# Performance work log

Hardware: AMD Instinct MI355X
Metric: run time of the kernel (lower is better)

Reference implementation:

```python
import jax, jax.numpy as jnp
import numpy as np

ROUTING_ITERS = 3
EPS = 1e-9


def squash(s):
    # s: [..., D]; faithful to the torch code: x / (1 + n^2) / sqrt(n^2 + eps)
    sq = jnp.sum(s * s, axis=-1, keepdims=True)
    return s / (1.0 + sq) / jnp.sqrt(sq + EPS)


def setup_inputs() -> dict:
    key = jax.random.key(0)
    k1, k2 = jax.random.split(key)
    B, I, C, D, d = 64, 4096, 32, 16, 16
    x = jax.random.normal(k1, (B, I, d), dtype=jnp.float32)
    weights = jax.random.normal(k2, (1, I, C, D, d), dtype=jnp.float32)
    return {"x": x, "weights": weights}


def reference(x, weights):
    # u_hat[b,i,c,D] = weights[0,i,c,D,d] @ x[b,i,d]
    u_hat = jnp.einsum('icDd,bid->bicD', weights[0], x)  # [B, I, C, D]
    B, I, C, D = u_hat.shape
    b_ij = jnp.zeros((B, I, C), dtype=u_hat.dtype)
    v_j = None
    for _ in range(ROUTING_ITERS):
        c_ij = jax.nn.softmax(b_ij, axis=2)                     # [B, I, C]
        s_j = jnp.einsum('bic,bicD->bcD', c_ij, u_hat)          # [B, C, D]
        v_j = squash(s_j)                                       # [B, C, D]
        b_ij = b_ij + jnp.einsum('bicD,bcD->bic', u_hat, v_j)   # agreement
    return v_j
```

## Files before the change

kernel.cpp:

```cpp
#include <hip/hip_runtime.h>
#include <math.h>

#define ITILES 256
#define IPB    16

typedef __bf16 bf16x8 __attribute__((ext_vector_type(8)));
typedef float  f32x16 __attribute__((ext_vector_type(16)));

__device__ inline unsigned short f2bf(float f) {
    unsigned int x = __float_as_uint(f);
    x += 0x7fff + ((x >> 16) & 1);
    return (unsigned short)(x >> 16);
}
__device__ inline float bf2f(unsigned short u) {
    return __uint_as_float(((unsigned int)u) << 16);
}
__device__ inline uint4 pack8(const unsigned short* o) {
    uint4 p;
    p.x = o[0] | ((unsigned)o[1] << 16);
    p.y = o[2] | ((unsigned)o[3] << 16);
    p.z = o[4] | ((unsigned)o[5] << 16);
    p.w = o[6] | ((unsigned)o[7] << 16);
    return p;
}

__device__ inline unsigned cvtpk(float lo, float hi) {
    unsigned r;
    asm("v_cvt_pk_bf16_f32 %0, %1, %2" : "=v"(r) : "v"(lo), "v"(hi));
    return r;
}
__device__ inline unsigned split3(float x, float y, unsigned& q2, unsigned& q3) {
    unsigned q1 = cvtpk(x, y);
    float f1x = __uint_as_float(q1 << 16);
    float f1y = __uint_as_float(q1 & 0xffff0000u);
    float rx = x - f1x, ry = y - f1y;
    q2 = cvtpk(rx, ry);
    float f2x = __uint_as_float(q2 << 16);
    float f2y = __uint_as_float(q2 & 0xffff0000u);
    q3 = cvtpk(rx - f2x, ry - f2y);
    return q1;
}

__global__ __launch_bounds__(128) void prep_x(const float* __restrict__ x,
                                              unsigned short* __restrict__ Xp)
{
    const int i = blockIdx.x;
    const int t = threadIdx.x;
    const int b = t >> 1, kh = t & 1;
    const float4* s4 = (const float4*)(x + ((size_t)b * 4096 + i) * 16 + kh * 8);
    float4 wa = s4[0], wb = s4[1];
    float wv[8] = {wa.x, wa.y, wa.z, wa.w, wb.x, wb.y, wb.z, wb.w};
    unsigned short o1[8], o2[8], o3[8];
    #pragma unroll
    for (int j = 0; j < 8; ++j) {
        float w = wv[j];
        o1[j] = f2bf(w);            float f1 = bf2f(o1[j]);
        o2[j] = f2bf(w - f1);       float f2 = bf2f(o2[j]);
        o3[j] = f2bf(w - f1 - f2);
    }
    unsigned short* dst = Xp + (size_t)i * 3072 + kh * 1536 + b * 8;
    *(uint4*)(dst)        = pack8(o1);
    *(uint4*)(dst + 512)  = pack8(o2);
    *(uint4*)(dst + 1024) = pack8(o3);
}

template<int USE_V>
__global__ __launch_bounds__(1024, 4)
void pass_kernel(const float* __restrict__ W,
                 const unsigned short* __restrict__ Xp,
                 const float* __restrict__ vg,
                 float* __restrict__ slab)
{
    __shared__ float4 vt[8192];
    __shared__ float  p_lds[32 * 65];
    __shared__ float  cij_lds[32 * 65];

    const int tid   = threadIdx.x;
    const int mt    = tid >> 6;
    const int lane  = tid & 63;
    const int l31   = lane & 31;
    const int h     = lane >> 5;
    const int cA    = 2 * mt + h;
    const int itile = blockIdx.x;
    const int i0    = itile * IPB;

    const int cW = 2 * mt + ((l31 >> 2) & 1);
    const int DW = (l31 & 3) + 4 * (l31 >> 3);
    const float4* w4 = (const float4*)(W + (size_t)i0 * 8192 + ((cW * 16 + DW) * 16 + h * 8));

    if (USE_V) {
        const float4* v4 = (const float4*)vg;
        #pragma unroll
        for (int k = 0; k < 8; ++k) {
            int idx = k * 1024 + tid;
            int b = idx >> 7, cd = idx & 127;
            vt[b * 128 + (cd ^ (b & 31))] = v4[idx];
        }
        __syncthreads();
    }

    f32x16 s0, s1;
    #pragma unroll
    for (int q = 0; q < 16; ++q) { s0[q] = 0.f; s1[q] = 0.f; }

    float4 wa = w4[0], wb = w4[1];

    for (int ii = 0; ii < IPB; ++ii) {
        const int i = i0 + ii;
        const unsigned short* bb = Xp + (size_t)i * 3072 + (size_t)h * 1536 + l31 * 8;

        uint4 b10 = *(const uint4*)(bb);
        uint4 b11 = *(const uint4*)(bb + 256);

        uint4 a1, a2, a3;
        a1.x = split3(wa.x, wa.y, a2.x, a3.x);
        a1.y = split3(wa.z, wa.w, a2.y, a3.y);
        a1.z = split3(wb.x, wb.y, a2.z, a3.z);
        a1.w = split3(wb.z, wb.w, a2.w, a3.w);

        {
            const int iin = (ii + 1 < IPB) ? (ii + 1) : ii;
            wa = w4[(size_t)iin * 2048];
            wb = w4[(size_t)iin * 2048 + 1];
        }

        #define MF(A_, B_, C_) __builtin_amdgcn_mfma_f32_32x32x16_bf16( \
            __builtin_bit_cast(bf16x8, A_), __builtin_bit_cast(bf16x8, B_), C_, 0, 0, 0)

        if (USE_V == 0) {
            s0 = MF(a1, b10, s0); s1 = MF(a1, b11, s1);
            uint4 b20 = *(const uint4*)(bb + 512);
            uint4 b21 = *(const uint4*)(bb + 512 + 256);
            s0 = MF(a2, b10, s0); s1 = MF(a2, b11, s1);
            uint4 b30 = *(const uint4*)(bb + 1024);
            uint4 b31 = *(const uint4*)(bb + 1024 + 256);
            s0 = MF(a1, b20, s0); s1 = MF(a1, b21, s1);
            s0 = MF(a3, b10, s0); s1 = MF(a3, b11, s1);
            s0 = MF(a2, b20, s0); s1 = MF(a2, b21, s1);
            s0 = MF(a1, b30, s0); s1 = MF(a1, b31, s1);
        } else {
            f32x16 u0, u1;
            #pragma unroll
            for (int q = 0; q < 16; ++q) { u0[q] = 0.f; u1[q] = 0.f; }
            u0 = MF(a1, b10, u0); u1 = MF(a1, b11, u1);
            uint4 b20 = *(const uint4*)(bb + 512);
            uint4 b21 = *(const uint4*)(bb + 512 + 256);
            u0 = MF(a2, b10, u0); u1 = MF(a2, b11, u1);
            uint4 b30 = *(const uint4*)(bb + 1024);
            uint4 b31 = *(const uint4*)(bb + 1024 + 256);
            u0 = MF(a1, b20, u0); u1 = MF(a1, b21, u1);
            u0 = MF(a3, b10, u0); u1 = MF(a3, b11, u1);
            u0 = MF(a2, b20, u0); u1 = MF(a2, b21, u1);
            u0 = MF(a1, b30, u0); u1 = MF(a1, b31, u1);

            #pragma unroll
            for (int nt = 0; nt < 2; ++nt) {
                const f32x16& uu = nt ? u1 : u0;
                const int b = nt * 32 + l31;
                float p = 0.f;
                #pragma unroll
                for (int dblk = 0; dblk < 4; ++dblk) {
                    float4 vv = vt[b * 128 + ((cA * 4 + dblk) ^ l31)];
                    p = fmaf(uu[dblk * 4 + 0], vv.x, p);
                    p = fmaf(uu[dblk * 4 + 1], vv.y, p);
                    p = fmaf(uu[dblk * 4 + 2], vv.z, p);
                    p = fmaf(uu[dblk * 4 + 3], vv.w, p);
                }
                p_lds[cA * 65 + b] = p;
            }
            __syncthreads();
            #pragma unroll
            for (int r2 = 0; r2 < 2; ++r2) {
                const int b = mt * 4 + r2 * 2 + h;
                float e = __expf(p_lds[l31 * 65 + b]);
                float t = e;
                t += __shfl_xor(t, 16); t += __shfl_xor(t, 8);
                t += __shfl_xor(t, 4);  t += __shfl_xor(t, 2);
                t += __shfl_xor(t, 1);
                cij_lds[l31 * 65 + b] = __fdividef(e, t);
            }
            __syncthreads();
            #pragma unroll
            for (int nt = 0; nt < 2; ++nt) {
                const f32x16& uu = nt ? u1 : u0;
                f32x16&       ss = nt ? s1 : s0;
                const int b = nt * 32 + l31;
                const float cij = cij_lds[cA * 65 + b];
                #pragma unroll
                for (int q = 0; q < 16; ++q) ss[q] = fmaf(cij, uu[q], ss[q]);
            }
        }
        #undef MF
    }

    float4* slab4 = (float4*)slab;
    #pragma unroll
    for (int nt = 0; nt < 2; ++nt) {
        const f32x16& ss = nt ? s1 : s0;
        const int b = nt * 32 + l31;
        size_t base = ((size_t)itile * 64 + b) * 128 + cA * 4;
        #pragma unroll
        for (int dblk = 0; dblk < 4; ++dblk) {
            float4 o = {ss[dblk * 4 + 0], ss[dblk * 4 + 1], ss[dblk * 4 + 2], ss[dblk * 4 + 3]};
            slab4[base + dblk] = o;
        }
    }
}

__global__ __launch_bounds__(256)
void reduce_squash(const float* __restrict__ slab, float* __restrict__ out, float scale,
                   const float* __restrict__ v1in, float* __restrict__ vsum)
{
    __shared__ float part[128];
    const int tid  = threadIdx.x;
    const int half = tid >> 7;
    const int o    = blockIdx.x * 128 + (tid & 127);
    float a[8];
    #pragma unroll
    for (int k = 0; k < 8; ++k) a[k] = 0.f;
    for (int g = 0; g < 16; ++g) {
        #pragma unroll
        for (int k = 0; k < 8; ++k)
            a[k] += slab[(size_t)(half * 128 + g * 8 + k) * 32768 + o];
    }
    float s = 0.f;
    #pragma unroll
    for (int k = 0; k < 8; ++k) s += a[k];
    if (half) part[tid & 127] = s;
    __syncthreads();
    if (!half) {
        s = (s + part[tid]) * scale;
        float t = s * s;
        t += __shfl_xor(t, 1);
        t += __shfl_xor(t, 2);
        t += __shfl_xor(t, 4);
        t += __shfl_xor(t, 8);
        float r = s / (1.0f + t) / sqrtf(t + 1e-9f);
        out[o] = r;
        if (v1in) vsum[o] = r + v1in[o];
    }
}

extern "C" void kernel_launch(void* const* d_in, const int* in_sizes, int n_in,
                              void* d_out, int out_size, void* d_ws, size_t ws_size,
                              hipStream_t stream)
{
    const float* x = (const float*)d_in[0];
    const float* W = (const float*)d_in[1];

    float* slab = (float*)d_ws;
    float* v1   = slab + (size_t)ITILES * 32768;
    float* v2   = v1 + 32768;
    float* v12  = v2 + 32768;
    unsigned short* Xp = (unsigned short*)(v12 + 32768);
    float* out  = (float*)d_out;

    hipLaunchKernelGGL(prep_x, dim3(4096), dim3(128), 0, stream, x, Xp);

    hipLaunchKernelGGL((pass_kernel<0>), dim3(ITILES), dim3(1024), 0, stream, W, Xp, (const float*)nullptr, slab);
    hipLaunchKernelGGL(reduce_squash,    dim3(256),    dim3(256),  0, stream, slab, v1, 1.0f / 32.0f, (const float*)nullptr, (float*)nullptr);
    hipLaunchKernelGGL((pass_kernel<1>), dim3(ITILES), dim3(1024), 0, stream, W, Xp, v1, slab);
    hipLaunchKernelGGL(reduce_squash,    dim3(256),    dim3(256),  0, stream, slab, v2, 1.0f, v1, v12);
    hipLaunchKernelGGL((pass_kernel<1>), dim3(ITILES), dim3(1024), 0, stream, W, Xp, v12, slab);
    hipLaunchKernelGGL(reduce_squash,    dim3(256),    dim3(256),  0, stream, slab, out, 1.0f, (const float*)nullptr, (float*)nullptr);
}
```

Measured before the change: 363.5 us.

## Split USE_V routing into per-half passes to cut live accumulators; add MFMA setprio

The agreement path now computes the u_hat tile for one 32-batch half at a time instead of holding both u0 and u1, which lowers register pressure. The dot-with-v, softmax and weighted accumulation run per half, so each half needs its own pair of barriers. The number of __syncthreads per i goes from two to four. It also hoists the B-operand loads ahead of the MFMA chains and wraps those chains in s_setprio to favour matrix issue across waves.

```diff
diff --git a/kernel.cpp b/kernel.cpp
--- a/kernel.cpp
+++ b/kernel.cpp
@@ -105,12 +105,12 @@
 
     float4 wa = w4[0], wb = w4[1];
 
+    #define MF(A_, B_, C_) __builtin_amdgcn_mfma_f32_32x32x16_bf16( \
+        __builtin_bit_cast(bf16x8, A_), __builtin_bit_cast(bf16x8, B_), C_, 0, 0, 0)
+
     for (int ii = 0; ii < IPB; ++ii) {
         const int i = i0 + ii;
         const unsigned short* bb = Xp + (size_t)i * 3072 + (size_t)h * 1536 + l31 * 8;
-
-        uint4 b10 = *(const uint4*)(bb);
-        uint4 b11 = *(const uint4*)(bb + 256);
 
         uint4 a1, a2, a3;
         a1.x = split3(wa.x, wa.y, a2.x, a3.x);
@@ -124,74 +124,77 @@
             wb = w4[(size_t)iin * 2048 + 1];
         }
 
-        #define MF(A_, B_, C_) __builtin_amdgcn_mfma_f32_32x32x16_bf16( \
-            __builtin_bit_cast(bf16x8, A_), __builtin_bit_cast(bf16x8, B_), C_, 0, 0, 0)
-
         if (USE_V == 0) {
-            s0 = MF(a1, b10, s0); s1 = MF(a1, b11, s1);
+            uint4 b10 = *(const uint4*)(bb);
+            uint4 b11 = *(const uint4*)(bb + 256);
             uint4 b20 = *(const uint4*)(bb + 512);
             uint4 b21 = *(const uint4*)(bb + 512 + 256);
+            __builtin_amdgcn_s_setprio(1);
+            s0 = MF(a1, b10, s0); s1 = MF(a1, b11, s1);
             s0 = MF(a2, b10, s0); s1 = MF(a2, b11, s1);
+            __builtin_amdgcn_s_setprio(0);
             uint4 b30 = *(const uint4*)(bb + 1024);
             uint4 b31 = *(const uint4*)(bb + 1024 + 256);
+            __builtin_amdgcn_s_setprio(1);
             s0 = MF(a1, b20, s0); s1 = MF(a1, b21, s1);
             s0 = MF(a3, b10, s0); s1 = MF(a3, b11, s1);
             s0 = MF(a2, b20, s0); s1 = MF(a2, b21, s1);
             s0 = MF(a1, b30, s0); s1 = MF(a1, b31, s1);
+            __builtin_amdgcn_s_setprio(0);
         } else {
-            f32x16 u0, u1;
-            #pragma unroll
-            for (int q = 0; q < 16; ++q) { u0[q] = 0.f; u1[q] = 0.f; }
-            u0 = MF(a1, b10, u0); u1 = MF(a1, b11, u1);
-            uint4 b20 = *(const uint4*)(bb + 512);
-            uint4 b21 = *(const uint4*)(bb + 512 + 256);
-            u0 = MF(a2, b10, u0); u1 = MF(a2, b11, u1);
-            uint4 b30 = *(const uint4*)(bb + 1024);
-            uint4 b31 = *(const uint4*)(bb + 1024 + 256);
-            u0 = MF(a1, b20, u0); u1 = MF(a1, b21, u1);
-            u0 = MF(a3, b10, u0); u1 = MF(a3, b11, u1);
-            u0 = MF(a2, b20, u0); u1 = MF(a2, b21, u1);
-            u0 = MF(a1, b30, u0); u1 = MF(a1, b31, u1);
-
             #pragma unroll
             for (int nt = 0; nt < 2; ++nt) {
-                const f32x16& uu = nt ? u1 : u0;
+                const unsigned short* bp = bb + nt * 256;
+                uint4 b1 = *(const uint4*)(bp);
+                uint4 b2 = *(const uint4*)(bp + 512);
+                uint4 b3 = *(const uint4*)(bp + 1024);
+
+                f32x16 u;
+                #pragma unroll
+                for (int q = 0; q < 16; ++q) u[q] = 0.f;
+                __builtin_amdgcn_s_setprio(1);
+                u = MF(a1, b1, u);
+                u = MF(a2, b1, u);
+                u = MF(a1, b2, u);
+                u = MF(a3, b1, u);
+                u = MF(a2, b2, u);
+                u = MF(a1, b3, u);
+                __builtin_amdgcn_s_setprio(0);
+
                 const int b = nt * 32 + l31;
                 float p = 0.f;
                 #pragma unroll
                 for (int dblk = 0; dblk < 4; ++dblk) {
                     float4 vv = vt[b * 128 + ((cA * 4 + dblk) ^ l31)];
-                    p = fmaf(uu[dblk * 4 + 0], vv.x, p);
-                    p = fmaf(uu[dblk * 4 + 1], vv.y, p);
-                    p = fmaf(uu[dblk * 4 + 2], vv.z, p);
-                    p = fmaf(uu[dblk * 4 + 3], vv.w, p);
+                    p = fmaf(u[dblk * 4 + 0], vv.x, p);
+                    p = fmaf(u[dblk * 4 + 1], vv.y, p);
+                    p = fmaf(u[dblk * 4 + 2], vv.z, p);
+                    p = fmaf(u[dblk * 4 + 3], vv.w, p);
                 }
                 p_lds[cA * 65 + b] = p;
+                __syncthreads();
+
+                {
+                    const int bsm = nt * 32 + mt * 2 + h;
+                    float e = __expf(p_lds[l31 * 65 + bsm]);
+                    float t = e;
+                    t += __shfl_xor(t, 16); t += __shfl_xor(t, 8);
+                    t += __shfl_xor(t, 4);  t += __shfl_xor(t, 2);
+                    t += __shfl_xor(t, 1);
+                    cij_lds[l31 * 65 + bsm] = __fdividef(e, t);
+                }
+                __syncthreads();
+
+                {
+                    f32x16& ss = nt ? s1 : s0;
+                    const float cij = cij_lds[cA * 65 + b];
+                    #pragma unroll
+                    for (int q = 0; q < 16; ++q) ss[q] = fmaf(cij, u[q], ss[q]);
+                }
             }
-            __syncthreads();
-            #pragma unroll
-            for (int r2 = 0; r2 < 2; ++r2) {
-                const int b = mt * 4 + r2 * 2 + h;
-                float e = __expf(p_lds[l31 * 65 + b]);
-                float t = e;
-                t += __shfl_xor(t, 16); t += __shfl_xor(t, 8);
-                t += __shfl_xor(t, 4);  t += __shfl_xor(t, 2);
-                t += __shfl_xor(t, 1);
-                cij_lds[l31 * 65 + b] = __fdividef(e, t);
-            }
-            __syncthreads();
-            #pragma unroll
-            for (int nt = 0; nt < 2; ++nt) {
-                const f32x16& uu = nt ? u1 : u0;
-                f32x16&       ss = nt ? s1 : s0;
-                const int b = nt * 32 + l31;
-                const float cij = cij_lds[cA * 65 + b];
-                #pragma unroll
-                for (int q = 0; q < 16; ++q) ss[q] = fmaf(cij, uu[q], ss[q]);
-            }
-        }
-        #undef MF
-    }
+        }
+    }
+    #undef MF
 
     float4* slab4 = (float4*)slab;
     #pragma unroll
```

After: 364.9 us. Within noise of the previous version (+0.4%).
